# Kernel tuning notes

Measured on AMD Instinct MI355X. Metric: run time of the kernel, lower is better.

## Reference

```python
import jax, jax.numpy as jnp
import numpy as np

N_CLASSES = 43
N_PRIM_CAPS = 8
PRIM_DIM = 16  # out channels per primary capsule conv
N_NODES = 16 * 9 * 9  # 1296
OUT_DIM = 16
N_ITER = 3
DN = ('NCHW', 'OIHW', 'NCHW')


def squash(v):
    # scale = |v|^2/(1+|v|^2); out = scale * v / |v|
    sn = jnp.sum(v * v, axis=-1, keepdims=True)
    return (sn / (1.0 + sn)) * v / jnp.sqrt(sn)


def setup_inputs() -> dict:
    key = jax.random.key(0)
    ks = jax.random.split(key, 6)
    x = jax.random.normal(ks[0], (64, 3, 32, 32), dtype=jnp.float32)
    conv1_w = 0.05 * jax.random.normal(ks[1], (256, 3, 9, 9), dtype=jnp.float32)
    conv1_b = 0.05 * jax.random.normal(ks[2], (256,), dtype=jnp.float32)
    # 8 independent Conv2d(256,16,8,stride=2) stacked capsule-major into one conv
    prim_w = 0.05 * jax.random.normal(ks[3], (N_PRIM_CAPS * PRIM_DIM, 256, 8, 8), dtype=jnp.float32)
    prim_b = 0.05 * jax.random.normal(ks[4], (N_PRIM_CAPS * PRIM_DIM,), dtype=jnp.float32)
    # route_weights: (1, n_nodes, n_caps, in_C=8, out_C=16); leading 1 dropped
    route_w = 0.1 * jax.random.normal(ks[5], (N_NODES, N_CLASSES, N_PRIM_CAPS, OUT_DIM), dtype=jnp.float32)
    return {"x": x, "conv1_w": conv1_w, "conv1_b": conv1_b,
            "prim_w": prim_w, "prim_b": prim_b, "route_w": route_w}


def reference(x, conv1_w, conv1_b, prim_w, prim_b, route_w):
    B = x.shape[0]
    # conv1 + relu: [B,3,32,32] -> [B,256,24,24]
    h = jax.lax.conv_general_dilated(x, conv1_w, (1, 1), 'VALID', dimension_numbers=DN)
    h = jax.nn.relu(h + conv1_b[None, :, None, None])
    # primary capsules: 8 convs fused -> [B,128,9,9]
    p = jax.lax.conv_general_dilated(h, prim_w, (2, 2), 'VALID', dimension_numbers=DN)
    p = p + prim_b[None, :, None, None]
    # per-capsule flatten (16*9*9=1296) then stack capsules on last axis -> [B,1296,8]
    p = p.reshape(B, N_PRIM_CAPS, N_NODES).transpose(0, 2, 1)
    u = squash(p)
    # priors: [B, n_nodes, n_classes, out_dim]
    priors = jnp.einsum('bni,ncio->bnco', u, route_w)
    logits = jnp.zeros_like(priors)
    outputs = None
    for i in range(N_ITER):
        probs = jax.nn.softmax(logits, axis=2)  # softmax over class axis
        outputs = squash(jnp.sum(probs * priors, axis=1, keepdims=True))  # [B,1,C,16]
        if i != N_ITER - 1:
            delta = jnp.sum(priors * outputs, axis=-1, keepdims=True)  # [B,n,C,1]
            logits = logits + delta  # broadcasts to [B,n,C,16]
    v = outputs[:, 0]  # [B,43,16]
    scores = jnp.sqrt(jnp.sum(v * v, axis=-1))  # [B,43]
    return scores
```

## Files before the change

### kernel.cpp

```cpp
#include <hip/hip_runtime.h>
#include <hip/hip_bf16.h>
#include <math.h>

static constexpr size_t W1T_OFF  = 0;
static constexpr size_t W2T_OFF  = 62208;
static constexpr size_t H_OFF    = 1110784;
static constexpr size_t PPART_OFF= 5829376;
static constexpr size_t UT_OFF   = 11137792;
static constexpr size_t S0_OFF   = 11801344;
static constexpr size_t OUT0_OFF = 11845376;
static constexpr size_t S1_OFF   = 11889408;
static constexpr size_t OUT1_OFF = 11933440;
static constexpr size_t S2_OFF   = 11977472;
static constexpr size_t PKW_OFF  = 0;
static constexpr size_t L_OFF    = 3698688;
static constexpr size_t PR_OFF   = 7265280;

typedef __bf16 bf16x8 __attribute__((ext_vector_type(8)));
typedef float  f32x4  __attribute__((ext_vector_type(4)));

__device__ inline unsigned pk2(float a, float b) {
    __hip_bfloat162 h = __float22bfloat162_rn(make_float2(a, b));
    return *(unsigned*)&h;
}

__global__ void k_init(float* ws) {
    int g = blockIdx.x * 256 + threadIdx.x;
    ws[S0_OFF + g] = 0.f;
}

__global__ void k_packb1(float* ws, const float* w1) {
    int g = blockIdx.x * 256 + threadIdx.x;
    int lane = g & 63;
    int r = g >> 6;
    int nt = r & 3, s = (r >> 2) % 14, ocq = r / 56;
    int quad = lane >> 4;
    int oc = ocq * 64 + nt * 16 + (lane & 15);
    int grp = 2 * s + (quad >> 1);
    int kxb = (quad & 1) * 8;
    uint4 o = {0u, 0u, 0u, 0u};
    if (grp < 27) {
        const float* wp = w1 + (size_t)oc * 243 + grp * 9;
        float v[8];
#pragma unroll
        for (int j = 0; j < 8; ++j) {
            int kx = kxb + j;
            v[j] = (kx < 9) ? wp[kx] : 0.f;
        }
        o.x = pk2(v[0], v[1]); o.y = pk2(v[2], v[3]);
        o.z = pk2(v[4], v[5]); o.w = pk2(v[6], v[7]);
    }
    ((uint4*)(ws + W1T_OFF))[g] = o;
}

__global__ void k_pack2(float* ws, const float* w2) {
    int g = blockIdx.x * 256 + threadIdx.x;
    int s = g >> 9;
    int r = g & 511;
    int nt = r >> 6, lane = r & 63;
    int n = nt * 16 + (lane & 15);
    int k0 = s * 32 + (lane >> 4) * 8;
    const float4* src = (const float4*)(w2 + (size_t)n * 16384 + k0);
    float4 v0 = src[0], v1 = src[1];
    uint4 o;
    o.x = pk2(v0.x, v0.y); o.y = pk2(v0.z, v0.w);
    o.z = pk2(v1.x, v1.y); o.w = pk2(v1.z, v1.w);
    ((uint4*)(ws + W2T_OFF))[g] = o;
}

__global__ void k_packw(float* ws, const float* rw) {
    int g = blockIdx.x * 256 + threadIdx.x;
    int lane = g & 63;
    int e = g >> 6;
    int c = e / 336;
    int r = e % 336;
    int tile = r / 21, ks = r % 21;
    int quad = lane >> 4, o = lane & 15;
    int nl = ks * 4 + quad;
    uint4 out = {0u, 0u, 0u, 0u};
    if (nl < 81) {
        int n = tile * 81 + nl;
        const float* wp = rw + ((size_t)n * 43 + c) * 128 + o;
        out.x = pk2(wp[0],  wp[16]);
        out.y = pk2(wp[32], wp[48]);
        out.z = pk2(wp[64], wp[80]);
        out.w = pk2(wp[96], wp[112]);
    }
    ((uint4*)(ws + PKW_OFF))[g] = out;
}

__global__ __launch_bounds__(256, 1) void k_conv1_mfma(float* ws, const float* x,
                                                       const float* b1) {
    __shared__ float xf[3136];
    __shared__ unsigned xd[2][1552];
    int blk = blockIdx.x;
    int b = blk >> 2, ocq = blk & 3;
    int t = threadIdx.x;

    const float4* xg = (const float4*)(x + (size_t)b * 3072);
    float4* xf4 = (float4*)xf;
#pragma unroll
    for (int i = t; i < 784; i += 256)
        xf4[i] = (i < 768) ? xg[i] : make_float4(0.f, 0.f, 0.f, 0.f);
    __syncthreads();
    for (int i = t; i < 1552; i += 256) {
        float a0 = xf[2 * i], a1 = xf[2 * i + 1], a2 = xf[2 * i + 2];
        xd[0][i] = pk2(a0, a1);
        xd[1][i] = pk2(a1, a2);
    }
    __syncthreads();

    int w = t >> 6, lane = t & 63;
    int quad = lane >> 4, mrow = lane & 15;

    f32x4 acc[9][4];
#pragma unroll
    for (int mt = 0; mt < 9; ++mt)
#pragma unroll
        for (int nt = 0; nt < 4; ++nt) acc[mt][nt] = (f32x4){0.f, 0.f, 0.f, 0.f};

    int exo[9];
#pragma unroll
    for (int mt = 0; mt < 9; ++mt) {
        int p = (w * 9 + mt) * 16 + mrow;
        exo[mt] = (p / 24) * 32 + (p % 24) + (quad & 1) * 8;
    }

    const uint4* pkb = (const uint4*)(ws + W1T_OFF) + (size_t)(ocq * 56) * 64;
    int gh = quad >> 1;

    for (int s = 0; s < 14; ++s) {
        int g = 2 * s + gh;
        int goff = (g < 27) ? (g / 9) * 1024 + (g % 9) * 32 : 0;
        uint4 bfr[4];
#pragma unroll
        for (int nt = 0; nt < 4; ++nt) bfr[nt] = pkb[(size_t)(s * 4 + nt) * 64 + lane];
        union { unsigned u[4]; bf16x8 v; } afr[9];
#pragma unroll
        for (int mt = 0; mt < 9; ++mt) {
            int e = goff + exo[mt];
            const unsigned* xp = &xd[e & 1][e >> 1];
            afr[mt].u[0] = xp[0]; afr[mt].u[1] = xp[1];
            afr[mt].u[2] = xp[2]; afr[mt].u[3] = xp[3];
        }
#pragma unroll
        for (int nt = 0; nt < 4; ++nt) {
            union { uint4 u; bf16x8 v; } bv; bv.u = bfr[nt];
#pragma unroll
            for (int mt = 0; mt < 9; ++mt)
                acc[mt][nt] = __builtin_amdgcn_mfma_f32_16x16x32_bf16(
                    afr[mt].v, bv.v, acc[mt][nt], 0, 0, 0);
        }
    }

    unsigned short* hb = (unsigned short*)(ws + H_OFF);
#pragma unroll
    for (int nt = 0; nt < 4; ++nt) {
        int oc = ocq * 64 + nt * 16 + mrow;
        float bias = b1[oc];
        unsigned* hp = (unsigned*)(hb + (size_t)(b * 256 + oc) * 576);
#pragma unroll
        for (int mt = 0; mt < 9; ++mt) {
            int p = (w * 9 + mt) * 16 + quad * 4;
            float v0 = fmaxf(acc[mt][nt][0] + bias, 0.f);
            float v1 = fmaxf(acc[mt][nt][1] + bias, 0.f);
            float v2 = fmaxf(acc[mt][nt][2] + bias, 0.f);
            float v3 = fmaxf(acc[mt][nt][3] + bias, 0.f);
            hp[(p >> 1) + 0] = pk2(v0, v1);
            hp[(p >> 1) + 1] = pk2(v2, v3);
        }
    }
}

__global__ __launch_bounds__(256, 4) void k_conv2_mfma(float* ws) {
    __shared__ unsigned short hs[2][2304];
    int blk = blockIdx.x;
    int b  = blk >> 4;
    int kq = (blk >> 1) & 7;
    int nh = blk & 1;
    int t = threadIdx.x;
    int w = t >> 6, lane = t & 63;
    int quad = lane >> 4, m = lane & 15;
    int mg = w >> 1, ng = w & 1;

    int aoy2[3], aox[3];
#pragma unroll
    for (int mi = 0; mi < 3; ++mi) {
        int p = (mg * 3 + mi) * 16 + m;
        if (p > 80) p = 0;
        aoy2[mi] = (p / 9) * 2;
        aox[mi] = p % 9;
    }

    const float4* hsg = (const float4*)((const unsigned short*)(ws + H_OFF)
                         + (size_t)(b * 256 + kq * 32) * 576);
    const uint4* wp = (const uint4*)(ws + W2T_OFF);
    int ntb = nh * 4 + ng * 2;

    f32x4 acc[3][2];
#pragma unroll
    for (int mi = 0; mi < 3; ++mi)
#pragma unroll
        for (int ni = 0; ni < 2; ++ni) acc[mi][ni] = (f32x4){0.f, 0.f, 0.f, 0.f};

    auto bidx = [&](int st, int cL, int ks, int ni) -> size_t {
        int s = (kq * 32 + st * 4 + cL) * 2 + ks;
        return (size_t)(s * 8 + ntb + ni) * 64 + lane;
    };

    ((float4*)&hs[0][0])[t] = hsg[t];
    if (t < 32) ((float4*)&hs[0][0])[256 + t] = hsg[256 + t];
    uint4 bc0 = wp[bidx(0, 0, 0, 0)], bc1 = wp[bidx(0, 0, 0, 1)];
    uint4 bc2 = wp[bidx(0, 0, 1, 0)], bc3 = wp[bidx(0, 0, 1, 1)];
    __syncthreads();

    for (int st = 0; st < 8; ++st) {
        float4 pre0, pre1;
        bool more = (st < 7);
        if (more) {
            pre0 = hsg[(st + 1) * 288 + t];
            if (t < 32) pre1 = hsg[(st + 1) * 288 + 256 + t];
        }
        const unsigned short* buf = &hs[st & 1][0];
#pragma unroll
        for (int cL = 0; cL < 4; ++cL) {
            int nst = (cL < 3) ? st : st + 1;
            int ncl = (cL < 3) ? cL + 1 : 0;
            bool pf = (nst < 8);
            uint4 bn0, bn1, bn2, bn3;
            if (pf) {
                bn0 = wp[bidx(nst, ncl, 0, 0)]; bn1 = wp[bidx(nst, ncl, 0, 1)];
                bn2 = wp[bidx(nst, ncl, 1, 0)]; bn3 = wp[bidx(nst, ncl, 1, 1)];
            }
            const unsigned short* cbuf = buf + cL * 576;
#pragma unroll
            for (int ks = 0; ks < 2; ++ks) {
                union { uint4 u; bf16x8 v; } bf0, bf1;
                bf0.u = ks ? bc2 : bc0;
                bf1.u = ks ? bc3 : bc1;
                int rowk = ks * 4 + quad;
#pragma unroll
                for (int mi = 0; mi < 3; ++mi) {
                    const unsigned int* ap =
                        (const unsigned int*)cbuf + (aoy2[mi] + rowk) * 12 + aox[mi];
                    union { unsigned int u[4]; bf16x8 v; } af;
                    af.u[0] = ap[0]; af.u[1] = ap[1]; af.u[2] = ap[2]; af.u[3] = ap[3];
                    acc[mi][0] = __builtin_amdgcn_mfma_f32_16x16x32_bf16(
                        af.v, bf0.v, acc[mi][0], 0, 0, 0);
                    acc[mi][1] = __builtin_amdgcn_mfma_f32_16x16x32_bf16(
                        af.v, bf1.v, acc[mi][1], 0, 0, 0);
                }
            }
            if (pf) { bc0 = bn0; bc1 = bn1; bc2 = bn2; bc3 = bn3; }
        }
        __syncthreads();
        if (more) {
            ((float4*)&hs[(st + 1) & 1][0])[t] = pre0;
            if (t < 32) ((float4*)&hs[(st + 1) & 1][0])[256 + t] = pre1;
        }
        __syncthreads();
    }

    float* pp = ws + PPART_OFF + ((size_t)(kq * 64 + b) * 81) * 128;
#pragma unroll
    for (int mi = 0; mi < 3; ++mi) {
#pragma unroll
        for (int ni = 0; ni < 2; ++ni) {
            int n = nh * 64 + (ng * 2 + ni) * 16 + m;
#pragma unroll
            for (int reg = 0; reg < 4; ++reg) {
                int p = (mg * 3 + mi) * 16 + quad * 4 + reg;
                if (p < 81) pp[(size_t)p * 128 + n] = acc[mi][ni][reg];
            }
        }
    }
}

__global__ void k_squash_u(float* ws, const float* prim_b) {
    __shared__ float vs[128];
    __shared__ float fac[16];
    int blk = blockIdx.x;
    int b = blk / 81, s = blk % 81;
    int n = threadIdx.x;
    const float* pp = ws + PPART_OFF;
    float v = prim_b[n];
#pragma unroll
    for (int kq = 0; kq < 8; ++kq)
        v += pp[((size_t)(kq * 64 + b) * 81 + s) * 128 + n];
    vs[n] = v;
    __syncthreads();
    if (n < 16) {
        float sn = 0.f;
#pragma unroll
        for (int i = 0; i < 8; ++i) { float tv = vs[i * 16 + n]; sn += tv * tv; }
        fac[n] = sqrtf(sn) / (1.f + sn);
    }
    __syncthreads();
    int i = n >> 4, d = n & 15;
    ws[UT_OFF + ((size_t)(d * 81 + s) * 64 + b) * 8 + i] = v * fac[d];
}

__global__ __launch_bounds__(256) void k_saccum_mfma(float* ws, const float* probs,
                                                     float* sdst) {
    int bx = blockIdx.x;
    int c = bx % 43, tile = bx / 43;
    int n0 = tile * 81;
    int t = threadIdx.x;
    int w = t >> 6, lane = t & 63;
    int quad = lane >> 4, m = lane & 15;
    int b = w * 16 + m;
    const float* ut = ws + UT_OFF;
    const uint4* pkw = (const uint4*)(ws + PKW_OFF)
                       + ((size_t)(c * 16 + tile) * 21) * 64 + lane;
    f32x4 acc = {0.f, 0.f, 0.f, 0.f};
#pragma unroll 7
    for (int ks = 0; ks < 21; ++ks) {
        int nl = ks * 4 + quad;
        union { uint4 u; bf16x8 v; } bf;
        bf.u = pkw[(size_t)ks * 64];
        union { unsigned u[4]; bf16x8 v; } af;
        af.u[0] = af.u[1] = af.u[2] = af.u[3] = 0u;
        if (nl < 81) {
            int n = n0 + nl;
            const float4* up = (const float4*)(ut + ((size_t)n * 64 + b) * 8);
            float4 u0 = up[0], u1 = up[1];
            float pv = probs ? probs[((size_t)n * 43 + c) * 64 + b] : 1.0f;
            af.u[0] = pk2(u0.x * pv, u0.y * pv);
            af.u[1] = pk2(u0.z * pv, u0.w * pv);
            af.u[2] = pk2(u1.x * pv, u1.y * pv);
            af.u[3] = pk2(u1.z * pv, u1.w * pv);
        }
        acc = __builtin_amdgcn_mfma_f32_16x16x32_bf16(af.v, bf.v, acc, 0, 0, 0);
    }
#pragma unroll
    for (int reg = 0; reg < 4; ++reg) {
        int bo = w * 16 + quad * 4 + reg;
        atomicAdd(sdst + ((size_t)bo * 43 + c) * 16 + m, acc[reg]);
    }
}

__global__ void k_outsquash(const float* s, float* ot, float scale) {
    int g = blockIdx.x * 256 + threadIdx.x;
    if (g >= 2752) return;
    int b = g / 43, c = g % 43;
    const float4* sp = (const float4*)(s + (size_t)g * 16);
    float v[16]; float sn = 0.f;
#pragma unroll
    for (int q = 0; q < 4; ++q) {
        float4 w = sp[q];
        v[q * 4] = w.x * scale; v[q * 4 + 1] = w.y * scale;
        v[q * 4 + 2] = w.z * scale; v[q * 4 + 3] = w.w * scale;
    }
#pragma unroll
    for (int j = 0; j < 16; ++j) sn += v[j] * v[j];
    float f = sqrtf(sn) / (1.f + sn);
    float4* op = (float4*)(ot + ((size_t)c * 64 + b) * 16);
#pragma unroll
    for (int q = 0; q < 4; ++q)
        op[q] = make_float4(v[q*4] * f, v[q*4+1] * f, v[q*4+2] * f, v[q*4+3] * f);
}

__global__ __launch_bounds__(256) void k_delta_mfma(float* ws, const float* outt,
                                                    float* L, float* P, int add) {
    __shared__ float ls[2752];
    int n = blockIdx.x, t = threadIdx.x;
    int w = t >> 6, lane = t & 63;
    int quad = lane >> 4, col = lane & 15;
    int b = w * 16 + col;

    union { unsigned u[4]; bf16x8 v; } bfrag;
    bfrag.u[0] = bfrag.u[1] = bfrag.u[2] = bfrag.u[3] = 0u;
    if (quad == 0) {
        const float4* up = (const float4*)(ws + UT_OFF + ((size_t)n * 64 + b) * 8);
        float4 u0 = up[0], u1 = up[1];
        bfrag.u[0] = pk2(u0.x, u0.y); bfrag.u[1] = pk2(u0.z, u0.w);
        bfrag.u[2] = pk2(u1.x, u1.y); bfrag.u[3] = pk2(u1.z, u1.w);
    }

    int tile = n / 81, nl = n % 81;
    int ks = nl >> 2, qpk = nl & 3;
    const uint4* pkw = (const uint4*)(ws + PKW_OFF);
    size_t abase = ((size_t)tile * 21 + ks) * 64 + qpk * 16 + col;
    const float4* ot4 = (const float4*)outt;
    size_t obase = (size_t)b * 4 + quad;

    uint4 a_cur = pkw[abase];
    float4 o_cur = ot4[obase];
    for (int c = 0; c < 43; ++c) {
        uint4 a_nxt; float4 o_nxt;
        if (c < 42) {
            a_nxt = pkw[abase + (size_t)(c + 1) * 21504];
            o_nxt = ot4[obase + (size_t)(c + 1) * 256];
        }
        union { uint4 u; bf16x8 v; } afrag; afrag.u = a_cur;
        f32x4 zero = {0.f, 0.f, 0.f, 0.f};
        f32x4 acc = __builtin_amdgcn_mfma_f32_16x16x32_bf16(afrag.v, bfrag.v, zero, 0, 0, 0);
        float val = acc[0] * o_cur.x + acc[1] * o_cur.y
                  + acc[2] * o_cur.z + acc[3] * o_cur.w;
        val += __shfl_xor(val, 16);
        val += __shfl_xor(val, 32);
        if (quad == 0) {
            size_t idx = ((size_t)n * 43 + c) * 64 + b;
            float nv;
            if (add) {
                nv = L[idx] + val;
            } else {
                nv = val;
                L[idx] = nv;
            }
            ls[c * 64 + b] = nv;
        }
        a_cur = a_nxt; o_cur = o_nxt;
    }

    __syncthreads();
    if (t < 64) {
        int bb = t;
        float m = -1e30f;
#pragma unroll
        for (int c = 0; c < 43; ++c) m = fmaxf(m, ls[c * 64 + bb]);
        float ssum = 0.f;
#pragma unroll
        for (int c = 0; c < 43; ++c) {
            float e = __expf(ls[c * 64 + bb] - m);
            ls[c * 64 + bb] = e;
            ssum += e;
        }
        float inv = 1.f / ssum;
        float* pp = P + (size_t)n * 2752 + bb;
#pragma unroll
        for (int c = 0; c < 43; ++c) pp[c * 64] = ls[c * 64 + bb] * inv;
    }
}

__global__ void k_scores(const float* s2, float* out) {
    int g = blockIdx.x * 256 + threadIdx.x;
    if (g >= 2752) return;
    const float4* sp = (const float4*)(s2 + (size_t)g * 16);
    float sn = 0.f;
#pragma unroll
    for (int q = 0; q < 4; ++q) {
        float4 w = sp[q];
        sn += w.x * w.x + w.y * w.y + w.z * w.z + w.w * w.w;
    }
    out[g] = sn / (1.f + sn);
}

extern "C" void kernel_launch(void* const* d_in, const int* in_sizes, int n_in,
                              void* d_out, int out_size, void* d_ws, size_t ws_size,
                              hipStream_t stream) {
    const float* x  = (const float*)d_in[0];
    const float* w1 = (const float*)d_in[1];
    const float* b1 = (const float*)d_in[2];
    const float* w2 = (const float*)d_in[3];
    const float* b2 = (const float*)d_in[4];
    const float* rw = (const float*)d_in[5];
    float* ws  = (float*)d_ws;
    float* out = (float*)d_out;

    k_init      <<<860,  256, 0, stream>>>(ws);
    k_packb1    <<<56,   256, 0, stream>>>(ws, w1);
    k_pack2     <<<1024, 256, 0, stream>>>(ws, w2);
    k_conv1_mfma<<<256,  256, 0, stream>>>(ws, x, b1);
    k_conv2_mfma<<<1024, 256, 0, stream>>>(ws);
    k_squash_u  <<<5184, 128, 0, stream>>>(ws, b2);
    k_packw     <<<3612, 256, 0, stream>>>(ws, rw);
    k_saccum_mfma<<<688, 256, 0, stream>>>(ws, nullptr, ws + S0_OFF);
    k_outsquash <<<11,  256, 0, stream>>>(ws + S0_OFF, ws + OUT0_OFF, 1.0f / 43.0f);
    k_delta_mfma<<<1296,256, 0, stream>>>(ws, ws + OUT0_OFF, ws + L_OFF, ws + PR_OFF, 0);
    k_saccum_mfma<<<688, 256, 0, stream>>>(ws, ws + PR_OFF, ws + S1_OFF);
    k_outsquash <<<11,  256, 0, stream>>>(ws + S1_OFF, ws + OUT1_OFF, 1.0f);
    k_delta_mfma<<<1296,256, 0, stream>>>(ws, ws + OUT1_OFF, ws + L_OFF, ws + PR_OFF, 1);
    k_saccum_mfma<<<688, 256, 0, stream>>>(ws, ws + PR_OFF, ws + S2_OFF);
    k_scores    <<<11,  256, 0, stream>>>(ws + S2_OFF, out);
}
```

Before: 259.5 us.

## Split conv2 output channels across more blocks and drop redundant barrier

The primary-capsule conv kernel now splits the 128 output channels four ways instead of two. Each wave computes one 16-column N tile instead of two, the grid doubles to 2048 blocks, and launch bounds allow 8 blocks per CU. This cuts accumulator registers and B-operand prefetch per thread, aiming for higher occupancy and more parallel blocks. The cost is that each block reloads the same activation slab into LDS and issues twice the LDS A-fragment reads per MFMA. It also removes the barrier before the double-buffer store, which is safe because the end-of-iteration barrier already orders the reuse of that buffer.

```diff
diff --git a/kernel.cpp b/kernel.cpp
--- a/kernel.cpp
+++ b/kernel.cpp
@@ -172,12 +172,12 @@
     }
 }
 
-__global__ __launch_bounds__(256, 4) void k_conv2_mfma(float* ws) {
+__global__ __launch_bounds__(256, 8) void k_conv2_mfma(float* ws) {
     __shared__ unsigned short hs[2][2304];
     int blk = blockIdx.x;
-    int b  = blk >> 4;
-    int kq = (blk >> 1) & 7;
-    int nh = blk & 1;
+    int b  = blk >> 5;
+    int kq = (blk >> 2) & 7;
+    int nh = blk & 3;
     int t = threadIdx.x;
     int w = t >> 6, lane = t & 63;
     int quad = lane >> 4, m = lane & 15;
@@ -195,23 +195,20 @@
     const float4* hsg = (const float4*)((const unsigned short*)(ws + H_OFF)
                          + (size_t)(b * 256 + kq * 32) * 576);
     const uint4* wp = (const uint4*)(ws + W2T_OFF);
-    int ntb = nh * 4 + ng * 2;
-
-    f32x4 acc[3][2];
-#pragma unroll
-    for (int mi = 0; mi < 3; ++mi)
-#pragma unroll
-        for (int ni = 0; ni < 2; ++ni) acc[mi][ni] = (f32x4){0.f, 0.f, 0.f, 0.f};
-
-    auto bidx = [&](int st, int cL, int ks, int ni) -> size_t {
+    int ntb = nh * 2 + ng;
+
+    f32x4 acc[3];
+#pragma unroll
+    for (int mi = 0; mi < 3; ++mi) acc[mi] = (f32x4){0.f, 0.f, 0.f, 0.f};
+
+    auto bidx = [&](int st, int cL, int ks) -> size_t {
         int s = (kq * 32 + st * 4 + cL) * 2 + ks;
-        return (size_t)(s * 8 + ntb + ni) * 64 + lane;
+        return (size_t)(s * 8 + ntb) * 64 + lane;
     };
 
     ((float4*)&hs[0][0])[t] = hsg[t];
     if (t < 32) ((float4*)&hs[0][0])[256 + t] = hsg[256 + t];
-    uint4 bc0 = wp[bidx(0, 0, 0, 0)], bc1 = wp[bidx(0, 0, 0, 1)];
-    uint4 bc2 = wp[bidx(0, 0, 1, 0)], bc3 = wp[bidx(0, 0, 1, 1)];
+    uint4 bc0 = wp[bidx(0, 0, 0)], bc1 = wp[bidx(0, 0, 1)];
     __syncthreads();
 
     for (int st = 0; st < 8; ++st) {
@@ -227,17 +224,16 @@
             int nst = (cL < 3) ? st : st + 1;
             int ncl = (cL < 3) ? cL + 1 : 0;
             bool pf = (nst < 8);
-            uint4 bn0, bn1, bn2, bn3;
+            uint4 bn0, bn1;
             if (pf) {
-                bn0 = wp[bidx(nst, ncl, 0, 0)]; bn1 = wp[bidx(nst, ncl, 0, 1)];
-                bn2 = wp[bidx(nst, ncl, 1, 0)]; bn3 = wp[bidx(nst, ncl, 1, 1)];
+                bn0 = wp[bidx(nst, ncl, 0)];
+                bn1 = wp[bidx(nst, ncl, 1)];
             }
             const unsigned short* cbuf = buf + cL * 576;
 #pragma unroll
             for (int ks = 0; ks < 2; ++ks) {
-                union { uint4 u; bf16x8 v; } bf0, bf1;
-                bf0.u = ks ? bc2 : bc0;
-                bf1.u = ks ? bc3 : bc1;
+                union { uint4 u; bf16x8 v; } bf;
+                bf.u = ks ? bc1 : bc0;
                 int rowk = ks * 4 + quad;
 #pragma unroll
                 for (int mi = 0; mi < 3; ++mi) {
@@ -245,15 +241,12 @@
                         (const unsigned int*)cbuf + (aoy2[mi] + rowk) * 12 + aox[mi];
                     union { unsigned int u[4]; bf16x8 v; } af;
                     af.u[0] = ap[0]; af.u[1] = ap[1]; af.u[2] = ap[2]; af.u[3] = ap[3];
-                    acc[mi][0] = __builtin_amdgcn_mfma_f32_16x16x32_bf16(
-                        af.v, bf0.v, acc[mi][0], 0, 0, 0);
-                    acc[mi][1] = __builtin_amdgcn_mfma_f32_16x16x32_bf16(
-                        af.v, bf1.v, acc[mi][1], 0, 0, 0);
+                    acc[mi] = __builtin_amdgcn_mfma_f32_16x16x32_bf16(
+                        af.v, bf.v, acc[mi], 0, 0, 0);
                 }
             }
-            if (pf) { bc0 = bn0; bc1 = bn1; bc2 = bn2; bc3 = bn3; }
-        }
-        __syncthreads();
+            if (pf) { bc0 = bn0; bc1 = bn1; }
+        }
         if (more) {
             ((float4*)&hs[(st + 1) & 1][0])[t] = pre0;
             if (t < 32) ((float4*)&hs[(st + 1) & 1][0])[256 + t] = pre1;
@@ -264,14 +257,11 @@
     float* pp = ws + PPART_OFF + ((size_t)(kq * 64 + b) * 81) * 128;
 #pragma unroll
     for (int mi = 0; mi < 3; ++mi) {
-#pragma unroll
-        for (int ni = 0; ni < 2; ++ni) {
-            int n = nh * 64 + (ng * 2 + ni) * 16 + m;
-#pragma unroll
-            for (int reg = 0; reg < 4; ++reg) {
-                int p = (mg * 3 + mi) * 16 + quad * 4 + reg;
-                if (p < 81) pp[(size_t)p * 128 + n] = acc[mi][ni][reg];
-            }
+        int n = ntb * 16 + m;
+#pragma unroll
+        for (int reg = 0; reg < 4; ++reg) {
+            int p = (mg * 3 + mi) * 16 + quad * 4 + reg;
+            if (p < 81) pp[(size_t)p * 128 + n] = acc[mi][reg];
         }
     }
 }
@@ -462,7 +452,7 @@
     k_packb1    <<<56,   256, 0, stream>>>(ws, w1);
     k_pack2     <<<1024, 256, 0, stream>>>(ws, w2);
     k_conv1_mfma<<<256,  256, 0, stream>>>(ws, x, b1);
-    k_conv2_mfma<<<1024, 256, 0, stream>>>(ws);
+    k_conv2_mfma<<<2048, 256, 0, stream>>>(ws);
     k_squash_u  <<<5184, 128, 0, stream>>>(ws, b2);
     k_packw     <<<3612, 256, 0, stream>>>(ws, rw);
     k_saccum_mfma<<<688, 256, 0, stream>>>(ws, nullptr, ws + S0_OFF);
```

Measured after the change: 275.0 us. 6.0% more time.
